# Kernel tuning notes

Measured on AMD Instinct MI355X. Metric: run time of the kernel, lower is better.

The kernel has to match this reference:

```python
import jax, jax.numpy as jnp
import numpy as np

N = 131072      # num nodes
T = 16          # tile (block) size, tile_rows == tile_cols
BR = N // T     # block rows = 8192
K = 8           # nonzero blocks per block-row
IN_F, HID, NCLS = 128, 256, 64
LN_EPS = 1e-5


def setup_inputs() -> dict:
    key = jax.random.key(0)
    ks = jax.random.split(key, 8)
    features = jax.random.normal(ks[0], (N, IN_F), dtype=jnp.float32)
    block_vals = jax.random.uniform(ks[1], (BR, K, T, T), dtype=jnp.float32) / (K * T)
    block_cols = jax.random.randint(ks[2], (BR, K), 0, BR, dtype=jnp.int32)
    W0 = jax.random.normal(ks[3], (IN_F, HID), dtype=jnp.float32) / np.sqrt(IN_F)
    W1 = jax.random.normal(ks[4], (HID, HID), dtype=jnp.float32) / np.sqrt(HID)
    W2 = jax.random.normal(ks[5], (HID, NCLS), dtype=jnp.float32) / np.sqrt(HID)
    return {
        "features": features,
        "block_vals": block_vals,
        "W0": W0, "b0": jnp.zeros((HID,), jnp.float32),
        "W1": W1, "b1": jnp.zeros((HID,), jnp.float32),
        "W2": W2, "b2": jnp.zeros((NCLS,), jnp.float32),
        "g0": jnp.ones((HID,), jnp.float32), "beta0": jnp.zeros((HID,), jnp.float32),
        "g1": jnp.ones((HID,), jnp.float32), "beta1": jnp.zeros((HID,), jnp.float32),
        "block_cols": block_cols,
    }


def bcsr_spmm(block_vals, block_cols, z):
    """Block-CSR sparse matmul: out = A @ z.
    block_vals: [BR, K, T, T], block_cols: [BR, K] (block-column ids), z: [N, F]."""
    f = z.shape[-1]
    zb = z.reshape(BR, T, f)[block_cols]          # gather column blocks -> [BR, K, T, F]
    out = jnp.einsum('bkrc,bkcf->brf', block_vals, zb)  # block GEMM + accumulate over K
    return out.reshape(N, f)


def layer_norm(x, g, b):
    mu = jnp.mean(x, axis=-1, keepdims=True)
    var = jnp.mean(jnp.square(x - mu), axis=-1, keepdims=True)
    return g * (x - mu) * jax.lax.rsqrt(var + LN_EPS) + b


def reference(features, block_vals, W0, b0, W1, b1, W2, b2,
              g0, beta0, g1, beta1, block_cols):
    # layer 0: h' = A @ (h W0) + b0 ; relu ; LayerNorm
    h = bcsr_spmm(block_vals, block_cols, features @ W0) + b0
    h = layer_norm(jax.nn.relu(h), g0, beta0)
    # layer 1
    h = bcsr_spmm(block_vals, block_cols, h @ W1) + b1
    h = layer_norm(jax.nn.relu(h), g1, beta1)
    # output layer (no activation/norm)
    h = bcsr_spmm(block_vals, block_cols, h @ W2) + b2
    return h
```

## Files before the change

kernel.cpp:

```cpp
#include <hip/hip_runtime.h>
#include <hip/hip_bf16.h>


typedef __bf16 bf16;
typedef bf16 bf16x8 __attribute__((ext_vector_type(8)));
typedef bf16 bf16x4 __attribute__((ext_vector_type(4)));
typedef float f32x4 __attribute__((ext_vector_type(4)));

#define N_NODES 131072
#define BRQ 8192
#define KNZ 8
#define IN_F 128
#define HID 256
#define NCLS 64

static __device__ __forceinline__ f32x4 mfma16(bf16x8 a, bf16x8 b, f32x4 c) {
  return __builtin_amdgcn_mfma_f32_16x16x32_bf16(a, b, c, 0, 0, 0);
}

static __device__ __forceinline__ bf16x8 load8(const bf16* p) {
  return *(const bf16x8*)p;
}
static __device__ __forceinline__ bf16x8 load8(const float* p) {
  f32x4 a0 = *(const f32x4*)p;
  f32x4 a1 = *(const f32x4*)(p + 4);
  bf16x8 r;
  r[0] = (bf16)a0[0]; r[1] = (bf16)a0[1]; r[2] = (bf16)a0[2]; r[3] = (bf16)a0[3];
  r[4] = (bf16)a1[0]; r[5] = (bf16)a1[1]; r[6] = (bf16)a1[2]; r[7] = (bf16)a1[3];
  return r;
}

__global__ void transpose_all(const float* __restrict__ W0, const float* __restrict__ W1,
                              const float* __restrict__ W2, bf16* __restrict__ w0t,
                              bf16* __restrict__ w1t, bf16* __restrict__ w2t) {
  int idx = blockIdx.x * 256 + threadIdx.x;
  if (idx < 32768) {
    int r = idx >> 8, c = idx & 255;
    w0t[c * 128 + r] = (bf16)W0[idx];
  } else if (idx < 98304) {
    int j = idx - 32768; int r = j >> 8, c = j & 255;
    w1t[c * 256 + r] = (bf16)W1[j];
  } else {
    int j = idx - 98304; int r = j >> 6, c = j & 63;
    w2t[c * 256 + r] = (bf16)W2[j];
  }
}

template<typename TA, int KIN, int FOUT, int GRID>
__global__ __launch_bounds__(256) void gemm_bt(const TA* __restrict__ X,
                                               const bf16* __restrict__ WT,
                                               bf16* __restrict__ Zbt) {
  constexpr int CG  = FOUT / 64;
  constexpr int KS  = KIN / 32;
  constexpr int RTS = GRID * 4 / CG;
  constexpr int NT  = BRQ / RTS;

  const int wave = threadIdx.x >> 6;
  const int lane = threadIdx.x & 63;
  const int l15  = lane & 15;
  const int quad = lane >> 4;
  const int gw   = blockIdx.x * 4 + wave;
  const int cg   = gw % CG;
  const int rt0  = gw / CG;

  const bf16* __restrict__ wbase = WT + (long)(cg * 64 + l15) * KIN + quad * 8;
  bf16x8 bfr[KS][4];
#pragma unroll
  for (int k = 0; k < KS; ++k)
#pragma unroll
    for (int t = 0; t < 4; ++t)
      bfr[k][t] = *(const bf16x8*)(wbase + t * (16 * KIN) + k * 32);

  const TA* __restrict__ xbase = X + (long)l15 * KIN + quad * 8;

  bf16x8 aw[2][KS];
#pragma unroll
  for (int k = 0; k < KS; ++k)
    aw[0][k] = load8(xbase + (long)rt0 * (16 * KIN) + k * 32);

#pragma unroll
  for (int it = 0; it < NT; ++it) {
    const int rt = rt0 + it * RTS;
    if (it + 1 < NT) {
      const long xoff = (long)(rt + RTS) * (16 * KIN);
#pragma unroll
      for (int k = 0; k < KS; ++k)
        aw[(it + 1) & 1][k] = load8(xbase + xoff + k * 32);
    }
    f32x4 acc[4] = {};
#pragma unroll
    for (int k = 0; k < KS; ++k)
#pragma unroll
      for (int t = 0; t < 4; ++t)
        acc[t] = mfma16(aw[it & 1][k], bfr[k][t], acc[t]);
#pragma unroll
    for (int t = 0; t < 4; ++t) {
      int col = cg * 64 + t * 16 + l15;
      bf16x4 v;
#pragma unroll
      for (int i = 0; i < 4; ++i) v[i] = (bf16)acc[t][i];
      *(bf16x4*)(Zbt + ((long)rt * FOUT + col) * 16 + quad * 4) = v;
    }
  }
}

__global__ __launch_bounds__(256) void spmm_ln(const float* __restrict__ Abv,
                                               const int*   __restrict__ Abc,
                                               const bf16*  __restrict__ Zbt,
                                               const float* __restrict__ bias,
                                               const float* __restrict__ gamma,
                                               const float* __restrict__ beta,
                                               bf16* __restrict__ H) {
  const int wave = threadIdx.x >> 6;
  const int lane = threadIdx.x & 63;
  const int l15  = lane & 15;
  const int quad = lane >> 4;
  const int b    = blockIdx.x * 2 + (wave >> 1);
  const int ch   = wave & 1;

  const int*   bc    = Abc + b * KNZ;
  const int    cst   = (quad & 1) * 8;
  const int    half  = quad >> 1;
  const float* abase = Abv + (long)b * (KNZ * 256) + l15 * 16 + cst;

  bf16x8 afr[4];
  long   zb[4];
#pragma unroll
  for (int kp = 0; kp < 4; ++kp) {
    int blk = 2 * kp + half;
    afr[kp] = load8(abase + blk * 256);
    zb[kp]  = (long)bc[blk] * (HID * 16) + cst;
  }
  bf16x8 bfr[4][8];
#pragma unroll
  for (int kp = 0; kp < 4; ++kp)
#pragma unroll
    for (int t = 0; t < 8; ++t) {
      int f = ch * 128 + t * 16 + l15;
      bfr[kp][t] = *(const bf16x8*)(Zbt + zb[kp] + f * 16);
    }

  f32x4 acc[8] = {};
#pragma unroll
  for (int kp = 0; kp < 4; ++kp)
#pragma unroll
    for (int t = 0; t < 8; ++t)
      acc[t] = mfma16(afr[kp], bfr[kp][t], acc[t]);

  float gv[8], bv[8];
#pragma unroll
  for (int t = 0; t < 8; ++t) {
    int f = ch * 128 + t * 16 + l15;
    gv[t] = gamma[f];
    bv[t] = beta[f];
  }
  float ps[4] = {0.f, 0.f, 0.f, 0.f}, pss[4] = {0.f, 0.f, 0.f, 0.f};
#pragma unroll
  for (int t = 0; t < 8; ++t) {
    float bi = bias[ch * 128 + t * 16 + l15];
#pragma unroll
    for (int i = 0; i < 4; ++i) {
      float v = acc[t][i] + bi;
      v = v > 0.f ? v : 0.f;
      acc[t][i] = v;
      ps[i] += v;
      pss[i] += v * v;
    }
  }
#pragma unroll
  for (int m = 1; m < 16; m <<= 1) {
#pragma unroll
    for (int i = 0; i < 4; ++i) {
      ps[i]  += __shfl_xor(ps[i], m, 64);
      pss[i] += __shfl_xor(pss[i], m, 64);
    }
  }
  __shared__ float S[4][16], SS[4][16];
  if (l15 == 0) {
#pragma unroll
    for (int i = 0; i < 4; ++i) {
      S[wave][quad * 4 + i]  = ps[i];
      SS[wave][quad * 4 + i] = pss[i];
    }
  }
  __syncthreads();
#pragma unroll
  for (int i = 0; i < 4; ++i) {
    int r = quad * 4 + i;
    float s    = S[wave][r] + S[wave ^ 1][r];
    float ss   = SS[wave][r] + SS[wave ^ 1][r];
    float mu   = s * (1.f / 256.f);
    float var  = ss * (1.f / 256.f) - mu * mu;
    float rstd = rsqrtf(var + 1e-5f);
    bf16* hrow = H + (long)(b * 16 + r) * HID;
#pragma unroll
    for (int t = 0; t < 8; ++t) {
      int f = ch * 128 + t * 16 + l15;
      float y = (acc[t][i] - mu) * rstd * gv[t] + bv[t];
      hrow[f] = (bf16)y;
    }
  }
}

__global__ __launch_bounds__(256) void spmm_out(const float* __restrict__ Abv,
                                                const int*   __restrict__ Abc,
                                                const bf16*  __restrict__ Zbt,
                                                const float* __restrict__ bias,
                                                float* __restrict__ out) {
  const int wave = threadIdx.x >> 6;
  const int b    = blockIdx.x * 4 + wave;
  const int lane = threadIdx.x & 63;
  const int l15  = lane & 15;
  const int quad = lane >> 4;

  const int*   bc    = Abc + b * KNZ;
  const int    cst   = (quad & 1) * 8;
  const int    half  = quad >> 1;
  const float* abase = Abv + (long)b * (KNZ * 256) + l15 * 16 + cst;

  bf16x8 afr[4];
  long   zb[4];
#pragma unroll
  for (int kp = 0; kp < 4; ++kp) {
    int blk = 2 * kp + half;
    afr[kp] = load8(abase + blk * 256);
    zb[kp]  = (long)bc[blk] * (NCLS * 16) + cst;
  }
  bf16x8 bfr[4][4];
#pragma unroll
  for (int kp = 0; kp < 4; ++kp)
#pragma unroll
    for (int t = 0; t < 4; ++t) {
      int f = t * 16 + l15;
      bfr[kp][t] = *(const bf16x8*)(Zbt + zb[kp] + f * 16);
    }

  f32x4 acc[4] = {};
#pragma unroll
  for (int kp = 0; kp < 4; ++kp)
#pragma unroll
    for (int t = 0; t < 4; ++t)
      acc[t] = mfma16(afr[kp], bfr[kp][t], acc[t]);

#pragma unroll
  for (int t = 0; t < 4; ++t) {
    int f = t * 16 + l15;
    float bi = bias[f];
#pragma unroll
    for (int i = 0; i < 4; ++i) {
      out[(long)(b * 16 + quad * 4 + i) * NCLS + f] = acc[t][i] + bi;
    }
  }
}

extern "C" void kernel_launch(void* const* d_in, const int* in_sizes, int n_in,
                              void* d_out, int out_size, void* d_ws, size_t ws_size,
                              hipStream_t stream) {
  const float* features = (const float*)d_in[0];
  const float* bvals    = (const float*)d_in[1];
  const float* W0       = (const float*)d_in[2];
  const float* b0       = (const float*)d_in[3];
  const float* W1       = (const float*)d_in[4];
  const float* b1       = (const float*)d_in[5];
  const float* W2       = (const float*)d_in[6];
  const float* b2       = (const float*)d_in[7];
  const float* g0       = (const float*)d_in[8];
  const float* beta0    = (const float*)d_in[9];
  const float* g1       = (const float*)d_in[10];
  const float* beta1    = (const float*)d_in[11];
  const int*   bcols    = (const int*)d_in[12];
  float* outp = (float*)d_out;

  bf16* zbt = (bf16*)d_ws;
  bf16* h   = zbt + (size_t)N_NODES * HID;

  bf16* w0t = (bf16*)d_out;
  bf16* w1t = w0t + IN_F * HID;
  bf16* w2t = w1t + HID * HID;

  transpose_all<<<dim3(448), dim3(256), 0, stream>>>(W0, W1, W2, w0t, w1t, w2t);

  gemm_bt<float, IN_F, HID, 1024><<<dim3(1024), dim3(256), 0, stream>>>(features, w0t, zbt);
  spmm_ln<<<dim3(BRQ / 2), dim3(256), 0, stream>>>(bvals, bcols, zbt, b0, g0, beta0, h);
  gemm_bt<bf16, HID, HID, 1024><<<dim3(1024), dim3(256), 0, stream>>>(h, w1t, zbt);
  spmm_ln<<<dim3(BRQ / 2), dim3(256), 0, stream>>>(bvals, bcols, zbt, b1, g1, beta1, h);
  gemm_bt<bf16, HID, NCLS, 512><<<dim3(512), dim3(256), 0, stream>>>(h, w2t, zbt);
  spmm_out<<<dim3(BRQ / 4), dim3(256), 0, stream>>>(bvals, bcols, zbt, b2, outp);
}
```

Measured before the change: 462.7 us.

## Make spmm_ln persistent over four block-rows with software-pipelined gathers

Each spmm_ln workgroup now handles four consecutive block-row pairs instead of one. While the MFMAs for the current block-row run, it prefetches the next block-row's column indices, A-block values and gathered Z tiles, with sched_barriers fixing the order. Shared-memory reduction buffers are double-buffered by iteration parity so a single barrier per iteration is enough. The gain is meant to come from hiding gather latency and amortising launch overhead. The cost is higher register pressure (launch_bounds 256,2) and a quarter as many workgroups, which reduces the parallelism available to hide latency.

```diff
diff --git a/kernel.cpp b/kernel.cpp
--- a/kernel.cpp
+++ b/kernel.cpp
@@ -14,6 +14,8 @@
 #define HID 256
 #define NCLS 64
 
+#define SB() __builtin_amdgcn_sched_barrier(0)
+
 static __device__ __forceinline__ f32x4 mfma16(bf16x8 a, bf16x8 b, f32x4 c) {
   return __builtin_amdgcn_mfma_f32_16x16x32_bf16(a, b, c, 0, 0, 0);
 }
@@ -21,13 +23,16 @@
 static __device__ __forceinline__ bf16x8 load8(const bf16* p) {
   return *(const bf16x8*)p;
 }
-static __device__ __forceinline__ bf16x8 load8(const float* p) {
-  f32x4 a0 = *(const f32x4*)p;
-  f32x4 a1 = *(const f32x4*)(p + 4);
+static __device__ __forceinline__ bf16x8 cvt8(f32x4 a0, f32x4 a1) {
   bf16x8 r;
   r[0] = (bf16)a0[0]; r[1] = (bf16)a0[1]; r[2] = (bf16)a0[2]; r[3] = (bf16)a0[3];
   r[4] = (bf16)a1[0]; r[5] = (bf16)a1[1]; r[6] = (bf16)a1[2]; r[7] = (bf16)a1[3];
   return r;
+}
+static __device__ __forceinline__ bf16x8 load8(const float* p) {
+  f32x4 a0 = *(const f32x4*)p;
+  f32x4 a1 = *(const f32x4*)(p + 4);
+  return cvt8(a0, a1);
 }
 
 __global__ void transpose_all(const float* __restrict__ W0, const float* __restrict__ W1,
@@ -104,101 +109,165 @@
   }
 }
 
-__global__ __launch_bounds__(256) void spmm_ln(const float* __restrict__ Abv,
-                                               const int*   __restrict__ Abc,
-                                               const bf16*  __restrict__ Zbt,
-                                               const float* __restrict__ bias,
-                                               const float* __restrict__ gamma,
-                                               const float* __restrict__ beta,
-                                               bf16* __restrict__ H) {
+#define NITER 4
+
+__global__ __launch_bounds__(256, 2) void spmm_ln(const float* __restrict__ Abv,
+                                                  const int*   __restrict__ Abc,
+                                                  const bf16*  __restrict__ Zbt,
+                                                  const float* __restrict__ bias,
+                                                  const float* __restrict__ gamma,
+                                                  const float* __restrict__ beta,
+                                                  bf16* __restrict__ H) {
   const int wave = threadIdx.x >> 6;
   const int lane = threadIdx.x & 63;
   const int l15  = lane & 15;
   const int quad = lane >> 4;
-  const int b    = blockIdx.x * 2 + (wave >> 1);
+  const int pair = wave >> 1;
   const int ch   = wave & 1;
-
-  const int*   bc    = Abc + b * KNZ;
-  const int    cst   = (quad & 1) * 8;
-  const int    half  = quad >> 1;
-  const float* abase = Abv + (long)b * (KNZ * 256) + l15 * 16 + cst;
-
-  bf16x8 afr[4];
-  long   zb[4];
-#pragma unroll
-  for (int kp = 0; kp < 4; ++kp) {
-    int blk = 2 * kp + half;
-    afr[kp] = load8(abase + blk * 256);
-    zb[kp]  = (long)bc[blk] * (HID * 16) + cst;
-  }
-  bf16x8 bfr[4][8];
-#pragma unroll
-  for (int kp = 0; kp < 4; ++kp)
+  const int cst  = (quad & 1) * 8;
+  const int half = quad >> 1;
+
+  __shared__ float S[2][4][16], SS[2][4][16];
+
+  const int b0 = blockIdx.x * (2 * NITER) + pair;
+  const char* zbase = (const char*)Zbt;
+  const unsigned foff = (unsigned)(ch * 128 + l15) * 32;
+
+  bf16x8   afr[4];
+  unsigned zoff[4];
+  {
+    const float* ab = Abv + (long)b0 * (KNZ * 256) + l15 * 16 + cst;
+    const int*   bc = Abc + b0 * KNZ;
+#pragma unroll
+    for (int kp = 0; kp < 4; ++kp) {
+      int blk = 2 * kp + half;
+      afr[kp]  = load8(ab + blk * 256);
+      zoff[kp] = (unsigned)bc[blk] * (HID * 16 * 2) + (unsigned)cst * 2;
+    }
+  }
+  bf16x8 buf0[16];
+#pragma unroll
+  for (int kp = 0; kp < 2; ++kp)
+#pragma unroll
+    for (int t = 0; t < 8; ++t)
+      buf0[kp * 8 + t] = *(const bf16x8*)(zbase + zoff[kp] + foff + (unsigned)t * 512);
+  SB();
+
+#pragma unroll
+  for (int it = 0; it < NITER; ++it) {
+    const int  b    = b0 + 2 * it;
+    const bool more = (it + 1 < NITER);
+
+    int bcn[4];
+    if (more) {
+      const int* bc = Abc + (b + 2) * KNZ;
+#pragma unroll
+      for (int kp = 0; kp < 4; ++kp) bcn[kp] = bc[2 * kp + half];
+    }
+    SB();
+    bf16x8 buf1[16];
+#pragma unroll
+    for (int kp = 2; kp < 4; ++kp)
+#pragma unroll
+      for (int t = 0; t < 8; ++t)
+        buf1[(kp - 2) * 8 + t] = *(const bf16x8*)(zbase + zoff[kp] + foff + (unsigned)t * 512);
+    SB();
+    f32x4 araw[4][2];
+    if (more) {
+      const float* ab = Abv + (long)(b + 2) * (KNZ * 256) + l15 * 16 + cst;
+#pragma unroll
+      for (int kp = 0; kp < 4; ++kp) {
+        const float* p = ab + (2 * kp + half) * 256;
+        araw[kp][0] = *(const f32x4*)p;
+        araw[kp][1] = *(const f32x4*)(p + 4);
+      }
+    }
+    SB();
+    f32x4 acc[8] = {};
+#pragma unroll
+    for (int kp = 0; kp < 2; ++kp)
+#pragma unroll
+      for (int t = 0; t < 8; ++t)
+        acc[t] = mfma16(afr[kp], buf0[kp * 8 + t], acc[t]);
+    SB();
+    if (more) {
+#pragma unroll
+      for (int kp = 0; kp < 4; ++kp)
+        zoff[kp] = (unsigned)bcn[kp] * (HID * 16 * 2) + (unsigned)cst * 2;
+#pragma unroll
+      for (int kp = 0; kp < 2; ++kp)
+#pragma unroll
+        for (int t = 0; t < 8; ++t)
+          buf0[kp * 8 + t] = *(const bf16x8*)(zbase + zoff[kp] + foff + (unsigned)t * 512);
+    }
+    SB();
+#pragma unroll
+    for (int kp = 0; kp < 2; ++kp)
+#pragma unroll
+      for (int t = 0; t < 8; ++t)
+        acc[t] = mfma16(afr[2 + kp], buf1[kp * 8 + t], acc[t]);
+    if (more) {
+#pragma unroll
+      for (int kp = 0; kp < 4; ++kp) afr[kp] = cvt8(araw[kp][0], araw[kp][1]);
+    }
+    SB();
+    float ps[4] = {0.f, 0.f, 0.f, 0.f}, pss[4] = {0.f, 0.f, 0.f, 0.f};
+#pragma unroll
+    for (int t = 0; t < 8; ++t) {
+      float bi = bias[ch * 128 + t * 16 + l15];
+#pragma unroll
+      for (int i = 0; i < 4; ++i) {
+        float v = acc[t][i] + bi;
+        v = v > 0.f ? v : 0.f;
+        acc[t][i] = v;
+        ps[i] += v;
+        pss[i] += v * v;
+      }
+    }
+#pragma unroll
+    for (int m = 1; m < 16; m <<= 1) {
+#pragma unroll
+      for (int i = 0; i < 4; ++i) {
+        ps[i]  += __shfl_xor(ps[i], m, 64);
+        pss[i] += __shfl_xor(pss[i], m, 64);
+      }
+    }
+    const int par = it & 1;
+    if (l15 == 0) {
+#pragma unroll
+      for (int i = 0; i < 4; ++i) {
+        S[par][wave][quad * 4 + i]  = ps[i];
+        SS[par][wave][quad * 4 + i] = pss[i];
+      }
+    }
+    __builtin_amdgcn_sched_barrier(0);
+    asm volatile("s_waitcnt lgkmcnt(0)" ::: "memory");
+    __builtin_amdgcn_s_barrier();
+    __builtin_amdgcn_sched_barrier(0);
+    float gv[8], bvv[8];
 #pragma unroll
     for (int t = 0; t < 8; ++t) {
       int f = ch * 128 + t * 16 + l15;
-      bfr[kp][t] = *(const bf16x8*)(Zbt + zb[kp] + f * 16);
-    }
-
-  f32x4 acc[8] = {};
-#pragma unroll
-  for (int kp = 0; kp < 4; ++kp)
-#pragma unroll
-    for (int t = 0; t < 8; ++t)
-      acc[t] = mfma16(afr[kp], bfr[kp][t], acc[t]);
-
-  float gv[8], bv[8];
-#pragma unroll
-  for (int t = 0; t < 8; ++t) {
-    int f = ch * 128 + t * 16 + l15;
-    gv[t] = gamma[f];
-    bv[t] = beta[f];
-  }
-  float ps[4] = {0.f, 0.f, 0.f, 0.f}, pss[4] = {0.f, 0.f, 0.f, 0.f};
-#pragma unroll
-  for (int t = 0; t < 8; ++t) {
-    float bi = bias[ch * 128 + t * 16 + l15];
+      gv[t]  = gamma[f];
+      bvv[t] = beta[f];
+    }
 #pragma unroll
     for (int i = 0; i < 4; ++i) {
-      float v = acc[t][i] + bi;
-      v = v > 0.f ? v : 0.f;
-      acc[t][i] = v;
-      ps[i] += v;
-      pss[i] += v * v;
-    }
-  }
-#pragma unroll
-  for (int m = 1; m < 16; m <<= 1) {
-#pragma unroll
-    for (int i = 0; i < 4; ++i) {
-      ps[i]  += __shfl_xor(ps[i], m, 64);
-      pss[i] += __shfl_xor(pss[i], m, 64);
-    }
-  }
-  __shared__ float S[4][16], SS[4][16];
-  if (l15 == 0) {
-#pragma unroll
-    for (int i = 0; i < 4; ++i) {
-      S[wave][quad * 4 + i]  = ps[i];
-      SS[wave][quad * 4 + i] = pss[i];
-    }
-  }
-  __syncthreads();
-#pragma unroll
-  for (int i = 0; i < 4; ++i) {
-    int r = quad * 4 + i;
-    float s    = S[wave][r] + S[wave ^ 1][r];
-    float ss   = SS[wave][r] + SS[wave ^ 1][r];
-    float mu   = s * (1.f / 256.f);
-    float var  = ss * (1.f / 256.f) - mu * mu;
-    float rstd = rsqrtf(var + 1e-5f);
-    bf16* hrow = H + (long)(b * 16 + r) * HID;
-#pragma unroll
-    for (int t = 0; t < 8; ++t) {
-      int f = ch * 128 + t * 16 + l15;
-      float y = (acc[t][i] - mu) * rstd * gv[t] + bv[t];
-      hrow[f] = (bf16)y;
-    }
+      int r = quad * 4 + i;
+      float s    = S[par][wave][r] + S[par][wave ^ 1][r];
+      float ss   = SS[par][wave][r] + SS[par][wave ^ 1][r];
+      float mu   = s * (1.f / 256.f);
+      float var  = ss * (1.f / 256.f) - mu * mu;
+      float rstd = rsqrtf(var + 1e-5f);
+      bf16* hrow = H + (long)(b * 16 + r) * HID;
+#pragma unroll
+      for (int t = 0; t < 8; ++t) {
+        int f = ch * 128 + t * 16 + l15;
+        float y = (acc[t][i] - mu) * rstd * gv[t] + bvv[t];
+        hrow[f] = (bf16)y;
+      }
+    }
+    SB();
   }
 }
 
@@ -281,9 +350,9 @@
   transpose_all<<<dim3(448), dim3(256), 0, stream>>>(W0, W1, W2, w0t, w1t, w2t);
 
   gemm_bt<float, IN_F, HID, 1024><<<dim3(1024), dim3(256), 0, stream>>>(features, w0t, zbt);
-  spmm_ln<<<dim3(BRQ / 2), dim3(256), 0, stream>>>(bvals, bcols, zbt, b0, g0, beta0, h);
+  spmm_ln<<<dim3(BRQ / (2 * NITER)), dim3(256), 0, stream>>>(bvals, bcols, zbt, b0, g0, beta0, h);
   gemm_bt<bf16, HID, HID, 1024><<<dim3(1024), dim3(256), 0, stream>>>(h, w1t, zbt);
-  spmm_ln<<<dim3(BRQ / 2), dim3(256), 0, stream>>>(bvals, bcols, zbt, b1, g1, beta1, h);
+  spmm_ln<<<dim3(BRQ / (2 * NITER)), dim3(256), 0, stream>>>(bvals, bcols, zbt, b1, g1, beta1, h);
   gemm_bt<bf16, HID, NCLS, 512><<<dim3(512), dim3(256), 0, stream>>>(h, w2t, zbt);
   spmm_out<<<dim3(BRQ / 4), dim3(256), 0, stream>>>(bvals, bcols, zbt, b2, outp);
 }
```

Result: no change. 463.9 us (+0.3%).

## Pipeline spmm_ln across block-rows with global-to-LDS DMA prefetch

Applied to the files above, without the earlier changes.

Each workgroup now processes 8 block-rows in a loop. Each of its four waves owns a 64-feature slice, and the next block-row's gathered Z tiles are prefetched into per-wave LDS buffers with global_load_lds while the current row's MFMA and LayerNorm run. Block-value loads are also prefetched into registers. The goal is to hide gather latency and cut per-row launch and redundancy overhead, at the cost of fewer workgroups, 64KB of LDS per block (lower occupancy), and per-row barriers.

```diff
diff --git a/kernel.cpp b/kernel.cpp
--- a/kernel.cpp
+++ b/kernel.cpp
@@ -14,6 +14,8 @@
 #define HID 256
 #define NCLS 64
 
+#define SB() __builtin_amdgcn_sched_barrier(0)
+
 static __device__ __forceinline__ f32x4 mfma16(bf16x8 a, bf16x8 b, f32x4 c) {
   return __builtin_amdgcn_mfma_f32_16x16x32_bf16(a, b, c, 0, 0, 0);
 }
@@ -21,13 +23,22 @@
 static __device__ __forceinline__ bf16x8 load8(const bf16* p) {
   return *(const bf16x8*)p;
 }
-static __device__ __forceinline__ bf16x8 load8(const float* p) {
-  f32x4 a0 = *(const f32x4*)p;
-  f32x4 a1 = *(const f32x4*)(p + 4);
+static __device__ __forceinline__ bf16x8 cvt8(f32x4 a0, f32x4 a1) {
   bf16x8 r;
   r[0] = (bf16)a0[0]; r[1] = (bf16)a0[1]; r[2] = (bf16)a0[2]; r[3] = (bf16)a0[3];
   r[4] = (bf16)a1[0]; r[5] = (bf16)a1[1]; r[6] = (bf16)a1[2]; r[7] = (bf16)a1[3];
   return r;
+}
+static __device__ __forceinline__ bf16x8 load8(const float* p) {
+  f32x4 a0 = *(const f32x4*)p;
+  f32x4 a1 = *(const f32x4*)(p + 4);
+  return cvt8(a0, a1);
+}
+
+static __device__ __forceinline__ void dma16(const char* gsrc, char* ldst) {
+  __builtin_amdgcn_global_load_lds(
+      (const __attribute__((address_space(1))) void*)gsrc,
+      (__attribute__((address_space(3))) void*)ldst, 16, 0, 0);
 }
 
 __global__ void transpose_all(const float* __restrict__ W0, const float* __restrict__ W1,
@@ -104,6 +115,8 @@
   }
 }
 
+#define RPW 8
+
 __global__ __launch_bounds__(256) void spmm_ln(const float* __restrict__ Abv,
                                                const int*   __restrict__ Abc,
                                                const bf16*  __restrict__ Zbt,
@@ -115,90 +128,133 @@
   const int lane = threadIdx.x & 63;
   const int l15  = lane & 15;
   const int quad = lane >> 4;
-  const int b    = blockIdx.x * 2 + (wave >> 1);
-  const int ch   = wave & 1;
-
-  const int*   bc    = Abc + b * KNZ;
-  const int    cst   = (quad & 1) * 8;
-  const int    half  = quad >> 1;
-  const float* abase = Abv + (long)b * (KNZ * 256) + l15 * 16 + cst;
-
-  bf16x8 afr[4];
-  long   zb[4];
-#pragma unroll
-  for (int kp = 0; kp < 4; ++kp) {
-    int blk = 2 * kp + half;
-    afr[kp] = load8(abase + blk * 256);
-    zb[kp]  = (long)bc[blk] * (HID * 16) + cst;
-  }
-  bf16x8 bfr[4][8];
-#pragma unroll
-  for (int kp = 0; kp < 4; ++kp)
-#pragma unroll
-    for (int t = 0; t < 8; ++t) {
-      int f = ch * 128 + t * 16 + l15;
-      bfr[kp][t] = *(const bf16x8*)(Zbt + zb[kp] + f * 16);
-    }
-
-  f32x4 acc[8] = {};
-#pragma unroll
-  for (int kp = 0; kp < 4; ++kp)
-#pragma unroll
-    for (int t = 0; t < 8; ++t)
-      acc[t] = mfma16(afr[kp], bfr[kp][t], acc[t]);
-
-  float gv[8], bv[8];
-#pragma unroll
-  for (int t = 0; t < 8; ++t) {
-    int f = ch * 128 + t * 16 + l15;
-    gv[t] = gamma[f];
-    bv[t] = beta[f];
-  }
-  float ps[4] = {0.f, 0.f, 0.f, 0.f}, pss[4] = {0.f, 0.f, 0.f, 0.f};
-#pragma unroll
-  for (int t = 0; t < 8; ++t) {
-    float bi = bias[ch * 128 + t * 16 + l15];
+  const int half = quad >> 1;
+  const int kb   = (quad & 1) * 16;
+
+  __shared__ __align__(16) char stage[4][16 * 1024];
+  __shared__ float S[2][4][16], SS[2][4][16];
+
+  char* wbuf = &stage[wave][0];
+  const char* zbase = (const char*)Zbt;
+  const unsigned fbyte = (unsigned)((wave * 64 + l15) * 32) + (unsigned)kb;
+
+  float bi[4], gv[4], bvv[4];
+#pragma unroll
+  for (int t = 0; t < 4; ++t) {
+    int f = wave * 64 + t * 16 + l15;
+    bi[t] = bias[f]; gv[t] = gamma[f]; bvv[t] = beta[f];
+  }
+
+  const int b0 = blockIdx.x * RPW;
+
+  f32x4 ar[4][2];
+  {
+    const int*   bc    = Abc + b0 * KNZ;
+    const float* abase = Abv + (long)b0 * (KNZ * 256) + l15 * 16 + (quad & 1) * 8;
+#pragma unroll
+    for (int kp = 0; kp < 4; ++kp) {
+      const char* src = zbase + (long)bc[2 * kp + half] * 8192 + fbyte;
+#pragma unroll
+      for (int t = 0; t < 4; ++t)
+        dma16(src + t * 512, wbuf + (kp * 4 + t) * 1024);
+      const float* p = abase + (2 * kp + half) * 256;
+      ar[kp][0] = *(const f32x4*)p;
+      ar[kp][1] = *(const f32x4*)(p + 4);
+    }
+  }
+
+#pragma unroll
+  for (int it = 0; it < RPW; ++it) {
+    const int b = b0 + it;
+
+    long zoffn[4];
+    const float* abn = Abv;
+    if (it + 1 < RPW) {
+      const int* bc = Abc + (b + 1) * KNZ;
+#pragma unroll
+      for (int kp = 0; kp < 4; ++kp)
+        zoffn[kp] = (long)bc[2 * kp + half] * 8192;
+      abn = Abv + (long)(b + 1) * (KNZ * 256) + l15 * 16 + (quad & 1) * 8;
+    }
+
+    asm volatile("s_waitcnt vmcnt(0)" ::: "memory");
+
+    bf16x8 afr[4];
+#pragma unroll
+    for (int kp = 0; kp < 4; ++kp) afr[kp] = cvt8(ar[kp][0], ar[kp][1]);
+
+    f32x4 acc[4] = {};
+#pragma unroll
+    for (int kp = 0; kp < 4; ++kp)
+#pragma unroll
+      for (int t = 0; t < 4; ++t) {
+        bf16x8 bf = *(const bf16x8*)(wbuf + (kp * 4 + t) * 1024 + lane * 16);
+        acc[t] = mfma16(afr[kp], bf, acc[t]);
+      }
+
+    SB();
+    if (it + 1 < RPW) {
+#pragma unroll
+      for (int kp = 0; kp < 4; ++kp) {
+        const char* src = zbase + zoffn[kp] + fbyte;
+#pragma unroll
+        for (int t = 0; t < 4; ++t)
+          dma16(src + t * 512, wbuf + (kp * 4 + t) * 1024);
+        const float* p = abn + (2 * kp + half) * 256;
+        ar[kp][0] = *(const f32x4*)p;
+        ar[kp][1] = *(const f32x4*)(p + 4);
+      }
+    }
+    SB();
+
+    float ps[4] = {0.f, 0.f, 0.f, 0.f}, pss[4] = {0.f, 0.f, 0.f, 0.f};
+#pragma unroll
+    for (int t = 0; t < 4; ++t)
+#pragma unroll
+      for (int i = 0; i < 4; ++i) {
+        float v = acc[t][i] + bi[t];
+        v = v > 0.f ? v : 0.f;
+        acc[t][i] = v;
+        ps[i] += v;
+        pss[i] += v * v;
+      }
+#pragma unroll
+    for (int m = 1; m < 16; m <<= 1) {
+#pragma unroll
+      for (int i = 0; i < 4; ++i) {
+        ps[i]  += __shfl_xor(ps[i], m, 64);
+        pss[i] += __shfl_xor(pss[i], m, 64);
+      }
+    }
+    const int par = it & 1;
+    if (l15 == 0) {
+#pragma unroll
+      for (int i = 0; i < 4; ++i) {
+        S[par][wave][quad * 4 + i]  = ps[i];
+        SS[par][wave][quad * 4 + i] = pss[i];
+      }
+    }
+    SB();
+    asm volatile("s_waitcnt lgkmcnt(0)" ::: "memory");
+    __builtin_amdgcn_s_barrier();
+    SB();
+
 #pragma unroll
     for (int i = 0; i < 4; ++i) {
-      float v = acc[t][i] + bi;
-      v = v > 0.f ? v : 0.f;
-      acc[t][i] = v;
-      ps[i] += v;
-      pss[i] += v * v;
-    }
-  }
-#pragma unroll
-  for (int m = 1; m < 16; m <<= 1) {
-#pragma unroll
-    for (int i = 0; i < 4; ++i) {
-      ps[i]  += __shfl_xor(ps[i], m, 64);
-      pss[i] += __shfl_xor(pss[i], m, 64);
-    }
-  }
-  __shared__ float S[4][16], SS[4][16];
-  if (l15 == 0) {
-#pragma unroll
-    for (int i = 0; i < 4; ++i) {
-      S[wave][quad * 4 + i]  = ps[i];
-      SS[wave][quad * 4 + i] = pss[i];
-    }
-  }
-  __syncthreads();
-#pragma unroll
-  for (int i = 0; i < 4; ++i) {
-    int r = quad * 4 + i;
-    float s    = S[wave][r] + S[wave ^ 1][r];
-    float ss   = SS[wave][r] + SS[wave ^ 1][r];
-    float mu   = s * (1.f / 256.f);
-    float var  = ss * (1.f / 256.f) - mu * mu;
-    float rstd = rsqrtf(var + 1e-5f);
-    bf16* hrow = H + (long)(b * 16 + r) * HID;
-#pragma unroll
-    for (int t = 0; t < 8; ++t) {
-      int f = ch * 128 + t * 16 + l15;
-      float y = (acc[t][i] - mu) * rstd * gv[t] + bv[t];
-      hrow[f] = (bf16)y;
-    }
+      int r = quad * 4 + i;
+      float s  = S[par][0][r] + S[par][1][r] + S[par][2][r] + S[par][3][r];
+      float ss = SS[par][0][r] + SS[par][1][r] + SS[par][2][r] + SS[par][3][r];
+      float mu   = s * (1.f / 256.f);
+      float var  = ss * (1.f / 256.f) - mu * mu;
+      float rstd = rsqrtf(var + 1e-5f);
+      bf16* hrow = H + (long)(b * 16 + r) * HID + wave * 64;
+#pragma unroll
+      for (int t = 0; t < 4; ++t) {
+        float y = (acc[t][i] - mu) * rstd * gv[t] + bvv[t];
+        hrow[t * 16 + l15] = (bf16)y;
+      }
+    }
+    SB();
   }
 }
 
@@ -281,9 +337,9 @@
   transpose_all<<<dim3(448), dim3(256), 0, stream>>>(W0, W1, W2, w0t, w1t, w2t);
 
   gemm_bt<float, IN_F, HID, 1024><<<dim3(1024), dim3(256), 0, stream>>>(features, w0t, zbt);
-  spmm_ln<<<dim3(BRQ / 2), dim3(256), 0, stream>>>(bvals, bcols, zbt, b0, g0, beta0, h);
+  spmm_ln<<<dim3(BRQ / RPW), dim3(256), 0, stream>>>(bvals, bcols, zbt, b0, g0, beta0, h);
   gemm_bt<bf16, HID, HID, 1024><<<dim3(1024), dim3(256), 0, stream>>>(h, w1t, zbt);
-  spmm_ln<<<dim3(BRQ / 2), dim3(256), 0, stream>>>(bvals, bcols, zbt, b1, g1, beta1, h);
+  spmm_ln<<<dim3(BRQ / RPW), dim3(256), 0, stream>>>(bvals, bcols, zbt, b1, g1, beta1, h);
   gemm_bt<bf16, HID, NCLS, 512><<<dim3(512), dim3(256), 0, stream>>>(h, w2t, zbt);
   spmm_out<<<dim3(BRQ / 4), dim3(256), 0, stream>>>(bvals, bcols, zbt, b2, outp);
 }
```

Measured after the change: 470.8 us. About the same (+1.8%).

## Reorder to aggregate-then-transform and fuse SpMM, GEMM, LayerNorm per layer

Applied to the files above, without the earlier changes.

Uses associativity, A(hW) = (Ah)W, so each layer first does the block-sparse aggregation on the narrower input features and then multiplies by W inside the same kernel. The aggregated tile is kept in shared memory as a bf16 hi/lo split to preserve precision, and bias, ReLU and LayerNorm are applied before a single write. The separate GEMM kernels and the Z intermediate round-trips are removed, and the next block-row's gathers are software-prefetched. The costs are doubled MFMA work for the hi/lo split, W held in registers (occupancy pressure), and a per-row block barrier.

```diff
diff --git a/kernel.cpp b/kernel.cpp
--- a/kernel.cpp
+++ b/kernel.cpp
@@ -13,243 +13,241 @@
 #define IN_F 128
 #define HID 256
 #define NCLS 64
+#define NROWS 8
+
+#define SB() __builtin_amdgcn_sched_barrier(0)
 
 static __device__ __forceinline__ f32x4 mfma16(bf16x8 a, bf16x8 b, f32x4 c) {
   return __builtin_amdgcn_mfma_f32_16x16x32_bf16(a, b, c, 0, 0, 0);
 }
 
-static __device__ __forceinline__ bf16x8 load8(const bf16* p) {
-  return *(const bf16x8*)p;
-}
-static __device__ __forceinline__ bf16x8 load8(const float* p) {
-  f32x4 a0 = *(const f32x4*)p;
-  f32x4 a1 = *(const f32x4*)(p + 4);
+static __device__ __forceinline__ bf16x8 cvt8(f32x4 a0, f32x4 a1) {
   bf16x8 r;
   r[0] = (bf16)a0[0]; r[1] = (bf16)a0[1]; r[2] = (bf16)a0[2]; r[3] = (bf16)a0[3];
   r[4] = (bf16)a1[0]; r[5] = (bf16)a1[1]; r[6] = (bf16)a1[2]; r[7] = (bf16)a1[3];
   return r;
 }
 
-__global__ void transpose_all(const float* __restrict__ W0, const float* __restrict__ W1,
-                              const float* __restrict__ W2, bf16* __restrict__ w0t,
-                              bf16* __restrict__ w1t, bf16* __restrict__ w2t) {
-  int idx = blockIdx.x * 256 + threadIdx.x;
-  if (idx < 32768) {
-    int r = idx >> 8, c = idx & 255;
-    w0t[c * 128 + r] = (bf16)W0[idx];
-  } else if (idx < 98304) {
-    int j = idx - 32768; int r = j >> 8, c = j & 255;
-    w1t[c * 256 + r] = (bf16)W1[j];
-  } else {
-    int j = idx - 98304; int r = j >> 6, c = j & 63;
-    w2t[c * 256 + r] = (bf16)W2[j];
-  }
-}
-
-template<typename TA, int KIN, int FOUT, int GRID>
-__global__ __launch_bounds__(256) void gemm_bt(const TA* __restrict__ X,
-                                               const bf16* __restrict__ WT,
-                                               bf16* __restrict__ Zbt) {
-  constexpr int CG  = FOUT / 64;
-  constexpr int KS  = KIN / 32;
-  constexpr int RTS = GRID * 4 / CG;
-  constexpr int NT  = BRQ / RTS;
+__global__ __launch_bounds__(256) void prep_fbt(const float* __restrict__ F,
+                                                bf16* __restrict__ out) {
+  __shared__ float T[16][132];
+  const int b = blockIdx.x, tid = threadIdx.x;
+#pragma unroll
+  for (int p = 0; p < 2; ++p) {
+    int ci = tid + p * 256;
+    int r = ci >> 5, c4 = ci & 31;
+    f32x4 v = *(const f32x4*)(F + ((long)b * 16 + r) * 128 + c4 * 4);
+    *(f32x4*)&T[r][c4 * 4] = v;
+  }
+  __syncthreads();
+  int f = tid >> 1, r0 = (tid & 1) * 8;
+  bf16x8 o;
+#pragma unroll
+  for (int e = 0; e < 8; ++e) o[e] = (bf16)T[r0 + e][f];
+  *(bf16x8*)(out + (long)b * 2048 + f * 16 + r0) = o;
+}
+
+template<int F_IN, int F_OUT, int WAVES, bool LN>
+__global__ __launch_bounds__(WAVES * 64, 2) void fused_layer(
+    const float* __restrict__ Abv, const int* __restrict__ Abc,
+    const bf16* __restrict__ Xbt, const float* __restrict__ W,
+    const float* __restrict__ bias, const float* __restrict__ gamma,
+    const float* __restrict__ beta, bf16* __restrict__ Hbt,
+    float* __restrict__ Out) {
+  constexpr int TS = F_IN / (16 * WAVES);
+  constexpr int TD = F_OUT / (16 * WAVES);
+  constexpr int KD = F_IN / 32;
+  constexpr int RW = F_IN + 8;
+  constexpr long XBLK = (long)F_IN * 32;
 
   const int wave = threadIdx.x >> 6;
   const int lane = threadIdx.x & 63;
-  const int l15  = lane & 15;
-  const int quad = lane >> 4;
-  const int gw   = blockIdx.x * 4 + wave;
-  const int cg   = gw % CG;
-  const int rt0  = gw / CG;
-
-  const bf16* __restrict__ wbase = WT + (long)(cg * 64 + l15) * KIN + quad * 8;
-  bf16x8 bfr[KS][4];
-#pragma unroll
-  for (int k = 0; k < KS; ++k)
-#pragma unroll
-    for (int t = 0; t < 4; ++t)
-      bfr[k][t] = *(const bf16x8*)(wbase + t * (16 * KIN) + k * 32);
-
-  const TA* __restrict__ xbase = X + (long)l15 * KIN + quad * 8;
-
-  bf16x8 aw[2][KS];
-#pragma unroll
-  for (int k = 0; k < KS; ++k)
-    aw[0][k] = load8(xbase + (long)rt0 * (16 * KIN) + k * 32);
-
-#pragma unroll
-  for (int it = 0; it < NT; ++it) {
-    const int rt = rt0 + it * RTS;
-    if (it + 1 < NT) {
-      const long xoff = (long)(rt + RTS) * (16 * KIN);
-#pragma unroll
-      for (int k = 0; k < KS; ++k)
-        aw[(it + 1) & 1][k] = load8(xbase + xoff + k * 32);
-    }
-    f32x4 acc[4] = {};
-#pragma unroll
-    for (int k = 0; k < KS; ++k)
-#pragma unroll
-      for (int t = 0; t < 4; ++t)
-        acc[t] = mfma16(aw[it & 1][k], bfr[k][t], acc[t]);
-#pragma unroll
-    for (int t = 0; t < 4; ++t) {
-      int col = cg * 64 + t * 16 + l15;
-      bf16x4 v;
-#pragma unroll
-      for (int i = 0; i < 4; ++i) v[i] = (bf16)acc[t][i];
-      *(bf16x4*)(Zbt + ((long)rt * FOUT + col) * 16 + quad * 4) = v;
-    }
-  }
-}
-
-__global__ __launch_bounds__(256) void spmm_ln(const float* __restrict__ Abv,
-                                               const int*   __restrict__ Abc,
-                                               const bf16*  __restrict__ Zbt,
-                                               const float* __restrict__ bias,
-                                               const float* __restrict__ gamma,
-                                               const float* __restrict__ beta,
-                                               bf16* __restrict__ H) {
-  const int wave = threadIdx.x >> 6;
-  const int lane = threadIdx.x & 63;
-  const int l15  = lane & 15;
-  const int quad = lane >> 4;
-  const int b    = blockIdx.x * 2 + (wave >> 1);
-  const int ch   = wave & 1;
-
-  const int*   bc    = Abc + b * KNZ;
-  const int    cst   = (quad & 1) * 8;
-  const int    half  = quad >> 1;
-  const float* abase = Abv + (long)b * (KNZ * 256) + l15 * 16 + cst;
-
-  bf16x8 afr[4];
-  long   zb[4];
-#pragma unroll
-  for (int kp = 0; kp < 4; ++kp) {
-    int blk = 2 * kp + half;
-    afr[kp] = load8(abase + blk * 256);
-    zb[kp]  = (long)bc[blk] * (HID * 16) + cst;
-  }
-  bf16x8 bfr[4][8];
-#pragma unroll
-  for (int kp = 0; kp < 4; ++kp)
-#pragma unroll
-    for (int t = 0; t < 8; ++t) {
-      int f = ch * 128 + t * 16 + l15;
-      bfr[kp][t] = *(const bf16x8*)(Zbt + zb[kp] + f * 16);
-    }
-
-  f32x4 acc[8] = {};
-#pragma unroll
-  for (int kp = 0; kp < 4; ++kp)
-#pragma unroll
-    for (int t = 0; t < 8; ++t)
-      acc[t] = mfma16(afr[kp], bfr[kp][t], acc[t]);
-
-  float gv[8], bv[8];
-#pragma unroll
-  for (int t = 0; t < 8; ++t) {
-    int f = ch * 128 + t * 16 + l15;
-    gv[t] = gamma[f];
-    bv[t] = beta[f];
-  }
-  float ps[4] = {0.f, 0.f, 0.f, 0.f}, pss[4] = {0.f, 0.f, 0.f, 0.f};
-#pragma unroll
-  for (int t = 0; t < 8; ++t) {
-    float bi = bias[ch * 128 + t * 16 + l15];
-#pragma unroll
-    for (int i = 0; i < 4; ++i) {
-      float v = acc[t][i] + bi;
-      v = v > 0.f ? v : 0.f;
-      acc[t][i] = v;
-      ps[i] += v;
-      pss[i] += v * v;
-    }
-  }
-#pragma unroll
-  for (int m = 1; m < 16; m <<= 1) {
-#pragma unroll
-    for (int i = 0; i < 4; ++i) {
-      ps[i]  += __shfl_xor(ps[i], m, 64);
-      pss[i] += __shfl_xor(pss[i], m, 64);
-    }
-  }
-  __shared__ float S[4][16], SS[4][16];
-  if (l15 == 0) {
-#pragma unroll
-    for (int i = 0; i < 4; ++i) {
-      S[wave][quad * 4 + i]  = ps[i];
-      SS[wave][quad * 4 + i] = pss[i];
-    }
-  }
-  __syncthreads();
-#pragma unroll
-  for (int i = 0; i < 4; ++i) {
-    int r = quad * 4 + i;
-    float s    = S[wave][r] + S[wave ^ 1][r];
-    float ss   = SS[wave][r] + SS[wave ^ 1][r];
-    float mu   = s * (1.f / 256.f);
-    float var  = ss * (1.f / 256.f) - mu * mu;
-    float rstd = rsqrtf(var + 1e-5f);
-    bf16* hrow = H + (long)(b * 16 + r) * HID;
-#pragma unroll
-    for (int t = 0; t < 8; ++t) {
-      int f = ch * 128 + t * 16 + l15;
-      float y = (acc[t][i] - mu) * rstd * gv[t] + bv[t];
-      hrow[f] = (bf16)y;
-    }
-  }
-}
-
-__global__ __launch_bounds__(256) void spmm_out(const float* __restrict__ Abv,
-                                                const int*   __restrict__ Abc,
-                                                const bf16*  __restrict__ Zbt,
-                                                const float* __restrict__ bias,
-                                                float* __restrict__ out) {
-  const int wave = threadIdx.x >> 6;
-  const int b    = blockIdx.x * 4 + wave;
-  const int lane = threadIdx.x & 63;
-  const int l15  = lane & 15;
-  const int quad = lane >> 4;
-
-  const int*   bc    = Abc + b * KNZ;
-  const int    cst   = (quad & 1) * 8;
-  const int    half  = quad >> 1;
-  const float* abase = Abv + (long)b * (KNZ * 256) + l15 * 16 + cst;
-
-  bf16x8 afr[4];
-  long   zb[4];
-#pragma unroll
-  for (int kp = 0; kp < 4; ++kp) {
-    int blk = 2 * kp + half;
-    afr[kp] = load8(abase + blk * 256);
-    zb[kp]  = (long)bc[blk] * (NCLS * 16) + cst;
-  }
-  bf16x8 bfr[4][4];
-#pragma unroll
-  for (int kp = 0; kp < 4; ++kp)
-#pragma unroll
-    for (int t = 0; t < 4; ++t) {
-      int f = t * 16 + l15;
-      bfr[kp][t] = *(const bf16x8*)(Zbt + zb[kp] + f * 16);
-    }
-
-  f32x4 acc[4] = {};
-#pragma unroll
-  for (int kp = 0; kp < 4; ++kp)
-#pragma unroll
-    for (int t = 0; t < 4; ++t)
-      acc[t] = mfma16(afr[kp], bfr[kp][t], acc[t]);
-
-#pragma unroll
-  for (int t = 0; t < 4; ++t) {
-    int f = t * 16 + l15;
-    float bi = bias[f];
-#pragma unroll
-    for (int i = 0; i < 4; ++i) {
-      out[(long)(b * 16 + quad * 4 + i) * NCLS + f] = acc[t][i] + bi;
-    }
+  const int l15 = lane & 15, quad = lane >> 4;
+  const int cst = (quad & 1) * 8, half = quad >> 1;
+  const int fsl = wave * 16 * TS;
+  const int nb  = wave * 16 * TD;
+
+  __shared__ bf16 Sh[2][16][RW];
+  __shared__ float LS[WAVES][16], LSS[WAVES][16];
+
+  bf16x8 wbf[KD][TD];
+#pragma unroll
+  for (int kp = 0; kp < KD; ++kp)
+#pragma unroll
+    for (int t = 0; t < TD; ++t) {
+      const float* wp = W + (long)(kp * 32 + quad * 8) * F_OUT + nb + t * 16 + l15;
+      bf16x8 v;
+#pragma unroll
+      for (int j = 0; j < 8; ++j) v[j] = (bf16)wp[(long)j * F_OUT];
+      wbf[kp][t] = v;
+    }
+  float bv[TD], gv[TD], btv[TD];
+#pragma unroll
+  for (int t = 0; t < TD; ++t) {
+    int n = nb + t * 16 + l15;
+    bv[t] = bias[n];
+    if constexpr (LN) { gv[t] = gamma[n]; btv[t] = beta[n]; }
+  }
+
+  const int b0 = blockIdx.x * NROWS;
+  const char* zb = (const char*)Xbt;
+  const unsigned fo0 = (unsigned)((fsl + l15) * 32 + cst * 2);
+
+  int bcc[4];
+  bf16x8 bfr[4][TS];
+  f32x4 araw[4][2];
+  {
+    const int* bc = Abc + b0 * KNZ;
+#pragma unroll
+    for (int kp = 0; kp < 4; ++kp) {
+      long zo = (long)bc[2 * kp + half] * XBLK;
+#pragma unroll
+      for (int t = 0; t < TS; ++t)
+        bfr[kp][t] = *(const bf16x8*)(zb + zo + fo0 + (unsigned)t * 512);
+    }
+    const float* ab = Abv + (long)b0 * (KNZ * 256) + l15 * 16 + cst;
+#pragma unroll
+    for (int kp = 0; kp < 4; ++kp) {
+      const float* p = ab + (2 * kp + half) * 256;
+      araw[kp][0] = *(const f32x4*)p;
+      araw[kp][1] = *(const f32x4*)(p + 4);
+    }
+    if (NROWS > 1) {
+      const int* bc1 = Abc + (b0 + 1) * KNZ;
+#pragma unroll
+      for (int kp = 0; kp < 4; ++kp) bcc[kp] = bc1[2 * kp + half];
+    }
+  }
+
+#pragma unroll
+  for (int it = 0; it < NROWS; ++it) {
+    const int b = b0 + it;
+    bf16x8 afr[4];
+#pragma unroll
+    for (int kp = 0; kp < 4; ++kp) afr[kp] = cvt8(araw[kp][0], araw[kp][1]);
+    int bcn[4];
+    if (it + 2 < NROWS) {
+      const int* bc = Abc + (b + 2) * KNZ;
+#pragma unroll
+      for (int kp = 0; kp < 4; ++kp) bcn[kp] = bc[2 * kp + half];
+    }
+    f32x4 sacc[TS] = {};
+#pragma unroll
+    for (int kp = 0; kp < 4; ++kp)
+#pragma unroll
+      for (int t = 0; t < TS; ++t)
+        sacc[t] = mfma16(afr[kp], bfr[kp][t], sacc[t]);
+    SB();
+#pragma unroll
+    for (int t = 0; t < TS; ++t) {
+      int f = fsl + t * 16 + l15;
+#pragma unroll
+      for (int i = 0; i < 4; ++i) {
+        float s = sacc[t][i];
+        bf16 hi = (bf16)s;
+        bf16 lo = (bf16)(s - (float)hi);
+        int r = quad * 4 + i;
+        Sh[0][r][f] = hi;
+        Sh[1][r][f] = lo;
+      }
+    }
+    SB();
+    if (it + 1 < NROWS) {
+#pragma unroll
+      for (int kp = 0; kp < 4; ++kp) {
+        long zo = (long)bcc[kp] * XBLK;
+#pragma unroll
+        for (int t = 0; t < TS; ++t)
+          bfr[kp][t] = *(const bf16x8*)(zb + zo + fo0 + (unsigned)t * 512);
+      }
+      const float* ab = Abv + (long)(b + 1) * (KNZ * 256) + l15 * 16 + cst;
+#pragma unroll
+      for (int kp = 0; kp < 4; ++kp) {
+        const float* p = ab + (2 * kp + half) * 256;
+        araw[kp][0] = *(const f32x4*)p;
+        araw[kp][1] = *(const f32x4*)(p + 4);
+      }
+      if (it + 2 < NROWS) {
+#pragma unroll
+        for (int kp = 0; kp < 4; ++kp) bcc[kp] = bcn[kp];
+      }
+    }
+    SB();
+    asm volatile("s_waitcnt lgkmcnt(0)" ::: "memory");
+    __builtin_amdgcn_s_barrier();
+    SB();
+    f32x4 dacc[TD] = {};
+#pragma unroll
+    for (int kp = 0; kp < KD; ++kp) {
+      bf16x8 shi = *(const bf16x8*)&Sh[0][l15][kp * 32 + quad * 8];
+      bf16x8 slo = *(const bf16x8*)&Sh[1][l15][kp * 32 + quad * 8];
+#pragma unroll
+      for (int t = 0; t < TD; ++t) {
+        dacc[t] = mfma16(shi, wbf[kp][t], dacc[t]);
+        dacc[t] = mfma16(slo, wbf[kp][t], dacc[t]);
+      }
+    }
+    SB();
+    if constexpr (LN) {
+      float ps[4] = {0.f, 0.f, 0.f, 0.f}, pss[4] = {0.f, 0.f, 0.f, 0.f};
+#pragma unroll
+      for (int t = 0; t < TD; ++t)
+#pragma unroll
+        for (int i = 0; i < 4; ++i) {
+          float v = dacc[t][i] + bv[t];
+          v = v > 0.f ? v : 0.f;
+          dacc[t][i] = v;
+          ps[i] += v;
+          pss[i] += v * v;
+        }
+#pragma unroll
+      for (int m = 1; m < 16; m <<= 1)
+#pragma unroll
+        for (int i = 0; i < 4; ++i) {
+          ps[i]  += __shfl_xor(ps[i], m, 64);
+          pss[i] += __shfl_xor(pss[i], m, 64);
+        }
+      if (l15 == 0)
+#pragma unroll
+        for (int i = 0; i < 4; ++i) {
+          LS[wave][quad * 4 + i]  = ps[i];
+          LSS[wave][quad * 4 + i] = pss[i];
+        }
+      SB();
+      asm volatile("s_waitcnt lgkmcnt(0)" ::: "memory");
+      __builtin_amdgcn_s_barrier();
+      SB();
+      float mu[4], rstd[4];
+#pragma unroll
+      for (int i = 0; i < 4; ++i) {
+        int r = quad * 4 + i;
+        float s = 0.f, ss = 0.f;
+#pragma unroll
+        for (int w = 0; w < WAVES; ++w) { s += LS[w][r]; ss += LSS[w][r]; }
+        mu[i] = s * (1.f / F_OUT);
+        float var = ss * (1.f / F_OUT) - mu[i] * mu[i];
+        rstd[i] = rsqrtf(var + 1e-5f);
+      }
+      bf16* hb = Hbt + (long)b * (F_OUT * 16);
+#pragma unroll
+      for (int t = 0; t < TD; ++t) {
+        int n = nb + t * 16 + l15;
+        bf16x4 o;
+#pragma unroll
+        for (int i = 0; i < 4; ++i)
+          o[i] = (bf16)((dacc[t][i] - mu[i]) * rstd[i] * gv[t] + btv[t]);
+        *(bf16x4*)(hb + n * 16 + quad * 4) = o;
+      }
+    } else {
+#pragma unroll
+      for (int t = 0; t < TD; ++t) {
+        int n = nb + t * 16 + l15;
+#pragma unroll
+        for (int i = 0; i < 4; ++i)
+          Out[((long)b * 16 + quad * 4 + i) * NCLS + n] = dacc[t][i] + bv[t];
+      }
+    }
+    SB();
   }
 }
 
@@ -271,19 +269,15 @@
   const int*   bcols    = (const int*)d_in[12];
   float* outp = (float*)d_out;
 
-  bf16* zbt = (bf16*)d_ws;
-  bf16* h   = zbt + (size_t)N_NODES * HID;
-
-  bf16* w0t = (bf16*)d_out;
-  bf16* w1t = w0t + IN_F * HID;
-  bf16* w2t = w1t + HID * HID;
-
-  transpose_all<<<dim3(448), dim3(256), 0, stream>>>(W0, W1, W2, w0t, w1t, w2t);
-
-  gemm_bt<float, IN_F, HID, 1024><<<dim3(1024), dim3(256), 0, stream>>>(features, w0t, zbt);
-  spmm_ln<<<dim3(BRQ / 2), dim3(256), 0, stream>>>(bvals, bcols, zbt, b0, g0, beta0, h);
-  gemm_bt<bf16, HID, HID, 1024><<<dim3(1024), dim3(256), 0, stream>>>(h, w1t, zbt);
-  spmm_ln<<<dim3(BRQ / 2), dim3(256), 0, stream>>>(bvals, bcols, zbt, b1, g1, beta1, h);
-  gemm_bt<bf16, HID, NCLS, 512><<<dim3(512), dim3(256), 0, stream>>>(h, w2t, zbt);
-  spmm_out<<<dim3(BRQ / 4), dim3(256), 0, stream>>>(bvals, bcols, zbt, b2, outp);
-}
+  bf16* fbt = (bf16*)d_ws;
+  bf16* hB  = (bf16*)d_ws;
+  bf16* hA  = (bf16*)d_ws + (size_t)N_NODES * HID;
+
+  prep_fbt<<<dim3(BRQ), dim3(256), 0, stream>>>(features, fbt);
+  fused_layer<IN_F, HID, 8, true><<<dim3(BRQ / NROWS), dim3(512), 0, stream>>>(
+      bvals, bcols, fbt, W0, b0, g0, beta0, hA, nullptr);
+  fused_layer<HID, HID, 8, true><<<dim3(BRQ / NROWS), dim3(512), 0, stream>>>(
+      bvals, bcols, hA, W1, b1, g1, beta1, hB, nullptr);
+  fused_layer<HID, NCLS, 4, false><<<dim3(BRQ / NROWS), dim3(256), 0, stream>>>(
+      bvals, bcols, hB, W2, b2, nullptr, nullptr, nullptr, outp);
+}
```

Result: no change. 463.9 us (+0.3%).
